# Optimization experiments

Hardware: AMD Instinct MI355X
Metric: run time of the kernel (lower is better)

## Reference

```python
import jax, jax.numpy as jnp
from jax import lax
import numpy as np

INPUT_SIZE, HIDDEN_SIZE, OUTPUT_SIZE = 256, 2048, 128
NUM_STEPS = 8192
ALPHA = 0.1


def setup_inputs() -> dict:
    key = jax.random.key(0)
    ks = jax.random.split(key, 8)
    s_i = 1.0 / np.sqrt(INPUT_SIZE)
    s_h = 1.0 / np.sqrt(HIDDEN_SIZE)
    return {
        "input_sig": jax.random.normal(ks[0], (INPUT_SIZE, NUM_STEPS), jnp.float32),
        "rate": jax.random.uniform(ks[1], (HIDDEN_SIZE,), jnp.float32, -1.0, 1.0),
        "Wi": jax.random.uniform(ks[2], (HIDDEN_SIZE, INPUT_SIZE), jnp.float32, -s_i, s_i),
        "bi": jax.random.uniform(ks[3], (HIDDEN_SIZE,), jnp.float32, -s_i, s_i),
        "Wh": jax.random.uniform(ks[4], (HIDDEN_SIZE, HIDDEN_SIZE), jnp.float32, -s_h, s_h),
        "bh": jax.random.uniform(ks[5], (HIDDEN_SIZE,), jnp.float32, -s_h, s_h),
        "Wo": jax.random.uniform(ks[6], (OUTPUT_SIZE, HIDDEN_SIZE), jnp.float32, -s_h, s_h),
        "bo": jax.random.uniform(ks[7], (OUTPUT_SIZE,), jnp.float32, -s_h, s_h),
    }


def reference(input_sig, rate, Wi, bi, Wh, bh, Wo, bo):
    # Precompute input projection for all steps at once: (T, H)
    xproj = input_sig.T @ Wi.T + bi  # einsum 'ti,hi->th'

    def step(r, xp):
        r_new = jnp.tanh(xp + r @ Wh.T + bh)
        r = (1.0 - ALPHA) * r + ALPHA * r_new
        return r, r

    _, rates = lax.scan(step, rate, xproj)  # rates: (T, H)
    rate_all = rates.T                      # (H, T), matches torch stack(dim=1)
    logits = rates @ Wo.T + bo              # (T, O)
    output = jax.nn.log_softmax(logits.T, axis=0)  # LogSoftmax over classes
    return output, rate_all
```

## Files before the change

### kernel.cpp

```cpp
#include <hip/hip_runtime.h>
#include <math.h>

#define T_STEPS 8192
#define HID     2048
#define IN_SZ   256
#define OUT_SZ  128
#define NBLK    128
#define NTHR    512
#define RPB     16
#define SCRUB   0xFFFFFFFF00000000ull

typedef unsigned long long u64;
typedef unsigned int u32;
typedef __attribute__((ext_vector_type(4))) u32 u32x4;


__global__ void k_init(const float* __restrict__ rate, u64* ring) {
    int i = blockIdx.x * blockDim.x + threadIdx.x;
    if (i < HID) {
        ring[i] = (u64)__float_as_uint(rate[i]);
        ring[HID + i]     = SCRUB;
        ring[2 * HID + i] = SCRUB;
    }
}

__global__ void __launch_bounds__(256) k_xproj(const float* __restrict__ sig,
                                               const float* __restrict__ Wi,
                                               const float* __restrict__ bi,
                                               float* __restrict__ out2) {
    __shared__ float wl[32 * IN_SZ];
    const int tid = threadIdx.x;
    const int t0 = blockIdx.x * 512;
    const int h0 = blockIdx.y * 32;

    {
        const float4* s4 = (const float4*)(Wi + (size_t)h0 * IN_SZ);
        float4* d4 = (float4*)wl;
        #pragma unroll
        for (int k = 0; k < 8; ++k) d4[tid + k * 256] = s4[tid + k * 256];
    }
    __syncthreads();

    const int t1 = t0 + tid, t2 = t1 + 256;
    float acc1[32], acc2[32];
    #pragma unroll
    for (int j = 0; j < 32; ++j) { acc1[j] = 0.f; acc2[j] = 0.f; }

    for (int i = 0; i < IN_SZ; ++i) {
        float s1 = sig[(size_t)i * T_STEPS + t1];
        float s2 = sig[(size_t)i * T_STEPS + t2];
        #pragma unroll
        for (int j = 0; j < 32; ++j) {
            float w = wl[j * IN_SZ + i];
            acc1[j] = fmaf(w, s1, acc1[j]);
            acc2[j] = fmaf(w, s2, acc2[j]);
        }
    }
    #pragma unroll
    for (int j = 0; j < 32; ++j) {
        float b = bi[h0 + j];
        out2[(size_t)(h0 + j) * T_STEPS + t1] = acc1[j] + b;
        out2[(size_t)(h0 + j) * T_STEPS + t2] = acc2[j] + b;
    }
}

__global__ void __launch_bounds__(512) k_scan(const float* __restrict__ Wh,
                                              const float* __restrict__ bh,
                                              float* __restrict__ out2,
                                              u64* ring) {
    __shared__ float whs[RPB * HID];
    __shared__ float rl[HID];
    const int tid  = threadIdx.x;
    const int bid  = blockIdx.x;
    const int w    = tid >> 6;
    const int lane = tid & 63;
    const int h0   = bid * RPB;
    const int ra   = h0 + 2 * w;
    const int rb   = ra + 1;

    {
        const float4* s4 = (const float4*)(Wh + (size_t)h0 * HID);
        float4* d4 = (float4*)whs;
        #pragma unroll
        for (int k = 0; k < RPB * HID / 4 / NTHR; ++k)
            d4[tid + k * NTHR] = s4[tid + k * NTHR];
    }
    const float bha = bh[ra], bhb = bh[rb];
    __syncthreads();

    int cur = 0;
    for (int t = 0; t < T_STEPS; ++t) {
        const size_t ia = (size_t)ra * T_STEPS + t;
        const size_t ib = (size_t)rb * T_STEPS + t;
        float xpa = 0.f, xpb = 0.f;
        if (lane == 0) { xpa = out2[ia]; xpb = out2[ib]; }

        {
            const u64* src = ring + (size_t)cur * HID;
            const u64* p0p = src + 4 * tid;
            const u64* p1p = p0p + 2;
            const u32 tt = (u32)t;
            u32x4 a0, a1;
            float f0, f1, f2, f3;
            int got = 0;
            for (int rounds = 0; rounds < 32; ++rounds) {
                asm volatile("global_load_dwordx4 %0, %2, off sc1\n\t"
                             "global_load_dwordx4 %1, %3, off sc1\n\t"
                             "s_waitcnt vmcnt(0)"
                             : "=&v"(a0), "=&v"(a1)
                             : "v"(p0p), "v"(p1p)
                             : "memory");
                __builtin_amdgcn_sched_barrier(0);
                if (a0.y == tt && a0.w == tt && a1.y == tt && a1.w == tt) {
                    f0 = __uint_as_float(a0.x);
                    f1 = __uint_as_float(a0.z);
                    f2 = __uint_as_float(a1.x);
                    f3 = __uint_as_float(a1.z);
                    got = 1;
                    break;
                }
            }
            if (!got) {
                u64 vals[4];
                unsigned pend = 0xFu;
                while (pend) {
                    #pragma unroll
                    for (int q = 0; q < 4; ++q) {
                        if (pend & (1u << q))
                            vals[q] = __hip_atomic_load(&p0p[q], __ATOMIC_RELAXED,
                                                        __HIP_MEMORY_SCOPE_AGENT);
                    }
                    #pragma unroll
                    for (int q = 0; q < 4; ++q) {
                        if ((pend & (1u << q)) && (u32)(vals[q] >> 32) == tt)
                            pend &= ~(1u << q);
                    }
                }
                f0 = __uint_as_float((u32)vals[0]);
                f1 = __uint_as_float((u32)vals[1]);
                f2 = __uint_as_float((u32)vals[2]);
                f3 = __uint_as_float((u32)vals[3]);
            }
            float4 v; v.x = f0; v.y = f1; v.z = f2; v.w = f3;
            ((float4*)rl)[tid] = v;
        }
        __syncthreads();

        float p0 = 0.f, p1 = 0.f;
        {
            const float4* r4 = (const float4*)rl;
            const float4* a4 = (const float4*)(whs + (size_t)(2 * w) * HID);
            const float4* b4 = (const float4*)(whs + (size_t)(2 * w + 1) * HID);
            #pragma unroll
            for (int c = 0; c < 8; ++c) {
                float4 rv = r4[c * 64 + lane];
                float4 av = a4[c * 64 + lane];
                float4 bv = b4[c * 64 + lane];
                p0 = fmaf(rv.x, av.x, p0); p0 = fmaf(rv.y, av.y, p0);
                p0 = fmaf(rv.z, av.z, p0); p0 = fmaf(rv.w, av.w, p0);
                p1 = fmaf(rv.x, bv.x, p1); p1 = fmaf(rv.y, bv.y, p1);
                p1 = fmaf(rv.z, bv.z, p1); p1 = fmaf(rv.w, bv.w, p1);
            }
        }
        #pragma unroll
        for (int off = 32; off >= 1; off >>= 1) {
            p0 += __shfl_xor(p0, off, 64);
            p1 += __shfl_xor(p1, off, 64);
        }

        const int nxt = (cur == 2) ? 0 : cur + 1;
        if (lane == 0) {
            float rolda = rl[ra];
            float roldb = rl[rb];
            float va = p0 + xpa + bha;
            float vb = p1 + xpb + bhb;
            float rna = 0.9f * rolda + 0.1f * tanhf(va);
            float rnb = 0.9f * roldb + 0.1f * tanhf(vb);
            out2[ia] = rna;
            out2[ib] = rnb;
            u64* dst = ring + (size_t)nxt * HID;
            const u64 tagbits = (u64)(u32)(t + 1) << 32;
            __hip_atomic_store(&dst[ra], tagbits | __float_as_uint(rna),
                               __ATOMIC_RELAXED, __HIP_MEMORY_SCOPE_AGENT);
            __hip_atomic_store(&dst[rb], tagbits | __float_as_uint(rnb),
                               __ATOMIC_RELAXED, __HIP_MEMORY_SCOPE_AGENT);
        }
        cur = nxt;
    }
}

__global__ void __launch_bounds__(512) k_logits(const float* __restrict__ out2,
                                                const float* __restrict__ Wo,
                                                const float* __restrict__ bo,
                                                float* __restrict__ out0) {
    __shared__ float wos[128 * 128];
    __shared__ float red[8 * 128];
    __shared__ float fin[128];
    const int tid  = threadIdx.x;
    const int w    = tid >> 6;
    const int lane = tid & 63;
    const int t0   = blockIdx.x * 128;
    const int ob   = w * 16;

    float acc0[16], acc1[16];
    #pragma unroll
    for (int j = 0; j < 16; ++j) { acc0[j] = 0.f; acc1[j] = 0.f; }

    for (int hb = 0; hb < HID / 128; ++hb) {
        __syncthreads();
        {
            const float4* wo4 = (const float4*)Wo;
            float4* ws4 = (float4*)wos;
            #pragma unroll
            for (int k = 0; k < 8; ++k) {
                int g = tid + k * 512;
                int o = g >> 5;
                int c = g & 31;
                ws4[g] = wo4[(size_t)o * (HID / 4) + hb * 32 + c];
            }
        }
        __syncthreads();
        for (int hh = 0; hh < 128; ++hh) {
            int h = hb * 128 + hh;
            float rA = out2[(size_t)h * T_STEPS + t0 + lane];
            float rB = out2[(size_t)h * T_STEPS + t0 + 64 + lane];
            #pragma unroll
            for (int j = 0; j < 16; ++j) {
                float wv = wos[(ob + j) * 128 + hh];
                acc0[j] = fmaf(wv, rA, acc0[j]);
                acc1[j] = fmaf(wv, rB, acc1[j]);
            }
        }
    }
    #pragma unroll
    for (int j = 0; j < 16; ++j) {
        float b = bo[ob + j];
        acc0[j] += b; acc1[j] += b;
    }

    float m0 = acc0[0], m1 = acc1[0];
    #pragma unroll
    for (int j = 1; j < 16; ++j) { m0 = fmaxf(m0, acc0[j]); m1 = fmaxf(m1, acc1[j]); }
    red[w * 128 + lane] = m0;
    red[w * 128 + 64 + lane] = m1;
    __syncthreads();
    if (tid < 128) {
        float m = red[tid];
        #pragma unroll
        for (int q = 1; q < 8; ++q) m = fmaxf(m, red[q * 128 + tid]);
        fin[tid] = m;
    }
    __syncthreads();
    float fm0 = fin[lane], fm1 = fin[64 + lane];
    float s0 = 0.f, s1 = 0.f;
    #pragma unroll
    for (int j = 0; j < 16; ++j) {
        s0 += expf(acc0[j] - fm0);
        s1 += expf(acc1[j] - fm1);
    }
    red[w * 128 + lane] = s0;
    red[w * 128 + 64 + lane] = s1;
    __syncthreads();
    if (tid < 128) {
        float s = 0.f;
        #pragma unroll
        for (int q = 0; q < 8; ++q) s += red[q * 128 + tid];
        fin[tid] = fin[tid] + logf(s);
    }
    __syncthreads();
    float L0 = fin[lane], L1 = fin[64 + lane];
    #pragma unroll
    for (int j = 0; j < 16; ++j) {
        out0[(size_t)(ob + j) * T_STEPS + t0 + lane]      = acc0[j] - L0;
        out0[(size_t)(ob + j) * T_STEPS + t0 + 64 + lane] = acc1[j] - L1;
    }
}

extern "C" void kernel_launch(void* const* d_in, const int* in_sizes, int n_in,
                              void* d_out, int out_size, void* d_ws, size_t ws_size,
                              hipStream_t stream) {
    const float* sig  = (const float*)d_in[0];
    const float* rate = (const float*)d_in[1];
    const float* Wi   = (const float*)d_in[2];
    const float* bi   = (const float*)d_in[3];
    const float* Wh   = (const float*)d_in[4];
    const float* bh   = (const float*)d_in[5];
    const float* Wo   = (const float*)d_in[6];
    const float* bo   = (const float*)d_in[7];

    float* out0 = (float*)d_out;
    float* out2 = out0 + (size_t)OUT_SZ * T_STEPS;

    u64* ring = (u64*)d_ws;

    hipLaunchKernelGGL(k_init, dim3(8), dim3(256), 0, stream, rate, ring);
    hipLaunchKernelGGL(k_xproj, dim3(T_STEPS / 512, HID / 32), dim3(256), 0, stream,
                       sig, Wi, bi, out2);

    void* args[] = {(void*)&Wh, (void*)&bh, (void*)&out2, (void*)&ring};
    hipLaunchCooperativeKernel((const void*)k_scan, dim3(NBLK), dim3(NTHR),
                               args, 0, stream);

    hipLaunchKernelGGL(k_logits, dim3(T_STEPS / 128), dim3(512), 0, stream,
                       out2, Wo, bo, out0);
}
```

Baseline: 16.60 ms.

## Hold recurrent weights in registers and halve the scan block count

The persistent scan kernel now keeps each wave's slice of Wh (four rows) in VGPRs instead of shared memory. This lets it run on 64 blocks with 32 rows each rather than 128 blocks with 16 rows. Fewer blocks means fewer participants in the per-step cross-block ring synchronisation, and the dot product no longer reads weights from LDS. The final tanh update is spread across four lanes. The cost is heavy register pressure (128 floats per lane for weights) with a risk of spills, and twice the FMA work per wave on each step.

```diff
diff --git a/kernel.cpp b/kernel.cpp
--- a/kernel.cpp
+++ b/kernel.cpp
@@ -5,9 +5,9 @@
 #define HID     2048
 #define IN_SZ   256
 #define OUT_SZ  128
-#define NBLK    128
+#define NBLK    64
 #define NTHR    512
-#define RPB     16
+#define RPB     32
 #define SCRUB   0xFFFFFFFF00000000ull
 
 typedef unsigned long long u64;
@@ -68,32 +68,36 @@
                                               const float* __restrict__ bh,
                                               float* __restrict__ out2,
                                               u64* ring) {
-    __shared__ float whs[RPB * HID];
     __shared__ float rl[HID];
     const int tid  = threadIdx.x;
     const int bid  = blockIdx.x;
     const int w    = tid >> 6;
     const int lane = tid & 63;
     const int h0   = bid * RPB;
-    const int ra   = h0 + 2 * w;
-    const int rb   = ra + 1;
-
+    const int ra   = h0 + 4 * w;
+
+    float4 wr[4][8];
     {
-        const float4* s4 = (const float4*)(Wh + (size_t)h0 * HID);
-        float4* d4 = (float4*)whs;
-        #pragma unroll
-        for (int k = 0; k < RPB * HID / 4 / NTHR; ++k)
-            d4[tid + k * NTHR] = s4[tid + k * NTHR];
-    }
-    const float bha = bh[ra], bhb = bh[rb];
+        const float4* Wh4 = (const float4*)Wh;
+        #pragma unroll
+        for (int j = 0; j < 4; ++j)
+            #pragma unroll
+            for (int c = 0; c < 8; ++c)
+                wr[j][c] = Wh4[(size_t)(ra + j) * (HID / 4) + c * 64 + lane];
+    }
+    const int myrow = ra + lane;
+    float mybh = 0.f;
+    if (lane < 4) mybh = bh[myrow];
     __syncthreads();
 
     int cur = 0;
     for (int t = 0; t < T_STEPS; ++t) {
-        const size_t ia = (size_t)ra * T_STEPS + t;
-        const size_t ib = (size_t)rb * T_STEPS + t;
-        float xpa = 0.f, xpb = 0.f;
-        if (lane == 0) { xpa = out2[ia]; xpb = out2[ib]; }
+        float xp = 0.f;
+        size_t myidx = 0;
+        if (lane < 4) {
+            myidx = (size_t)myrow * T_STEPS + t;
+            xp = out2[myidx];
+        }
 
         {
             const u64* src = ring + (size_t)cur * HID;
@@ -146,43 +150,41 @@
         }
         __syncthreads();
 
-        float p0 = 0.f, p1 = 0.f;
+        float p0 = 0.f, p1 = 0.f, p2 = 0.f, p3 = 0.f;
         {
             const float4* r4 = (const float4*)rl;
-            const float4* a4 = (const float4*)(whs + (size_t)(2 * w) * HID);
-            const float4* b4 = (const float4*)(whs + (size_t)(2 * w + 1) * HID);
             #pragma unroll
             for (int c = 0; c < 8; ++c) {
                 float4 rv = r4[c * 64 + lane];
-                float4 av = a4[c * 64 + lane];
-                float4 bv = b4[c * 64 + lane];
-                p0 = fmaf(rv.x, av.x, p0); p0 = fmaf(rv.y, av.y, p0);
-                p0 = fmaf(rv.z, av.z, p0); p0 = fmaf(rv.w, av.w, p0);
-                p1 = fmaf(rv.x, bv.x, p1); p1 = fmaf(rv.y, bv.y, p1);
-                p1 = fmaf(rv.z, bv.z, p1); p1 = fmaf(rv.w, bv.w, p1);
+                p0 = fmaf(rv.x, wr[0][c].x, p0); p0 = fmaf(rv.y, wr[0][c].y, p0);
+                p0 = fmaf(rv.z, wr[0][c].z, p0); p0 = fmaf(rv.w, wr[0][c].w, p0);
+                p1 = fmaf(rv.x, wr[1][c].x, p1); p1 = fmaf(rv.y, wr[1][c].y, p1);
+                p1 = fmaf(rv.z, wr[1][c].z, p1); p1 = fmaf(rv.w, wr[1][c].w, p1);
+                p2 = fmaf(rv.x, wr[2][c].x, p2); p2 = fmaf(rv.y, wr[2][c].y, p2);
+                p2 = fmaf(rv.z, wr[2][c].z, p2); p2 = fmaf(rv.w, wr[2][c].w, p2);
+                p3 = fmaf(rv.x, wr[3][c].x, p3); p3 = fmaf(rv.y, wr[3][c].y, p3);
+                p3 = fmaf(rv.z, wr[3][c].z, p3); p3 = fmaf(rv.w, wr[3][c].w, p3);
             }
         }
         #pragma unroll
         for (int off = 32; off >= 1; off >>= 1) {
             p0 += __shfl_xor(p0, off, 64);
             p1 += __shfl_xor(p1, off, 64);
+            p2 += __shfl_xor(p2, off, 64);
+            p3 += __shfl_xor(p3, off, 64);
         }
 
         const int nxt = (cur == 2) ? 0 : cur + 1;
-        if (lane == 0) {
-            float rolda = rl[ra];
-            float roldb = rl[rb];
-            float va = p0 + xpa + bha;
-            float vb = p1 + xpb + bhb;
-            float rna = 0.9f * rolda + 0.1f * tanhf(va);
-            float rnb = 0.9f * roldb + 0.1f * tanhf(vb);
-            out2[ia] = rna;
-            out2[ib] = rnb;
+        if (lane < 4) {
+            float myp = (lane & 2) ? ((lane & 1) ? p3 : p2)
+                                   : ((lane & 1) ? p1 : p0);
+            float rold = rl[myrow];
+            float v = myp + xp + mybh;
+            float rn = 0.9f * rold + 0.1f * tanhf(v);
+            out2[myidx] = rn;
             u64* dst = ring + (size_t)nxt * HID;
             const u64 tagbits = (u64)(u32)(t + 1) << 32;
-            __hip_atomic_store(&dst[ra], tagbits | __float_as_uint(rna),
-                               __ATOMIC_RELAXED, __HIP_MEMORY_SCOPE_AGENT);
-            __hip_atomic_store(&dst[rb], tagbits | __float_as_uint(rnb),
+            __hip_atomic_store(&dst[myrow], tagbits | __float_as_uint(rn),
                                __ATOMIC_RELAXED, __HIP_MEMORY_SCOPE_AGENT);
         }
         cur = nxt;
```

New measurement: 29.61 ms. 78.4% more time.
